# Optimization experiments

Measured on AMD Instinct MI355X. Metric: run time of the kernel, lower is better.

## Reference

```python
import jax, jax.numpy as jnp
import numpy as np

H = 256  # hidden_units
B = 64   # batch
D = 2048 # question length


def setup_inputs() -> dict:
    key = jax.random.key(0)
    ks = jax.random.split(key, 9)
    s = 1.0 / np.sqrt(H)
    return {
        "context": jax.random.normal(ks[0], (B, H), dtype=jnp.float32),
        "question": jax.random.normal(ks[1], (B, D, H), dtype=jnp.float32),
        "hidden": jax.random.normal(ks[2], (1, B, H), dtype=jnp.float32),
        "W1": jax.random.uniform(ks[3], (H, H), jnp.float32, -s, s),  # linear_g1, no bias
        "W2": jax.random.uniform(ks[4], (H, H), jnp.float32, -s, s),  # linear_g2
        "b2": jax.random.uniform(ks[5], (H,), jnp.float32, -s, s),
        "W3": jax.random.uniform(ks[6], (H, H), jnp.float32, -s, s),  # linear_g3, no bias
        "W4": jax.random.uniform(ks[7], (1, H), jnp.float32, -s, s),  # linear_g4
        "b4": jax.random.uniform(ks[8], (1,), jnp.float32, -s, s),
    }


def reference(context, question, hidden, W1, W2, b2, W3, W4, b4):
    # hidden: (1,B,H) -> (B,1,H); linear_g3 (no bias)
    g3 = jnp.swapaxes(hidden, 0, 1) @ W3.T            # (B,1,H)
    # linear_g2 on context, then unsqueeze(1)
    g2 = (context @ W2.T + b2)[:, None, :]            # (B,1,H)
    # linear_g1 on question (no bias)
    g1 = question @ W1.T                              # (B,D,H)
    # The torch repeat/view sequence is exactly a broadcast add in (B,D,H)
    s = jnp.tanh(g2 + g3 + g1)                        # (B,D,H)
    scores = s @ W4.T + b4                            # (B,D,1)
    attn = jax.nn.softmax(scores, axis=1)             # softmax over D
    # attn.transpose(1,2) bmm question -> (B,1,H)
    return jnp.einsum('bdo,bdh->boh', attn, question)
```

## Files before the change

kernel.cpp:

```cpp
#include <hip/hip_runtime.h>
#include <hip/hip_bf16.h>
#include <math.h>

#define HD 256
#define BB 64
#define DD 2048
#define NCHK 8
#define NST 4

typedef __attribute__((ext_vector_type(8))) short  short8;
typedef __attribute__((ext_vector_type(4))) float  float4v;
typedef __attribute__((ext_vector_type(4))) unsigned uint4v;
typedef __attribute__((ext_vector_type(4))) unsigned short ushort4v;

__device__ inline unsigned short f2bf(float f) {
    unsigned u = __builtin_bit_cast(unsigned, f);
    u += 0x7FFFu + ((u >> 16) & 1u);
    return (unsigned short)(u >> 16);
}
__device__ inline float bf2f(unsigned short u) {
    return __builtin_bit_cast(float, (unsigned)u << 16);
}

__device__ inline short8 cvt8(float4v lo, float4v hi) {
    uint4v u;
    asm("v_cvt_pk_bf16_f32 %0, %1, %2" : "=v"(u[0]) : "v"(lo[0]), "v"(lo[1]));
    asm("v_cvt_pk_bf16_f32 %0, %1, %2" : "=v"(u[1]) : "v"(lo[2]), "v"(lo[3]));
    asm("v_cvt_pk_bf16_f32 %0, %1, %2" : "=v"(u[2]) : "v"(hi[0]), "v"(hi[1]));
    asm("v_cvt_pk_bf16_f32 %0, %1, %2" : "=v"(u[3]) : "v"(hi[2]), "v"(hi[3]));
    return __builtin_bit_cast(short8, u);
}

__device__ inline float fast_exp2(float x) {
    float r;
    asm("v_exp_f32 %0, %1" : "=v"(r) : "v"(x));
    return r;
}
__device__ inline float fast_tanh(float x) {
    float y = x * 2.8853900817779268f;
    y = fminf(fmaxf(y, -30.f), 30.f);
    float t = fast_exp2(y);
    float r;
    asm("v_rcp_f32 %0, %1" : "=v"(r) : "v"(t + 1.f));
    return (t - 1.f) * r;
}

#define SYNC_LDS() do { asm volatile("s_waitcnt lgkmcnt(0)" ::: "memory"); \
                        __builtin_amdgcn_s_barrier(); \
                        asm volatile("" ::: "memory"); } while (0)

__global__ __launch_bounds__(256) void k_prep(const float* __restrict__ W1,
                                              unsigned short* __restrict__ w1b,
                                              const float* __restrict__ ctx,
                                              const float* __restrict__ hid,
                                              const float* __restrict__ W2,
                                              const float* __restrict__ b2,
                                              const float* __restrict__ W3,
                                              float* __restrict__ g23) {
    if (blockIdx.x < 64) {
        int i = blockIdx.x * 256 + threadIdx.x;
        float4v v = ((const float4v*)W1)[i];
        ushort4v o;
        o[0] = f2bf(v[0]); o[1] = f2bf(v[1]); o[2] = f2bf(v[2]); o[3] = f2bf(v[3]);
        ((ushort4v*)w1b)[i] = o;
    } else {
        int b = blockIdx.x - 64, t = threadIdx.x;
        __shared__ float c[HD], hh[HD];
        c[t]  = ctx[b * HD + t];
        hh[t] = hid[b * HD + t];
        __syncthreads();
        const float4v* w2 = (const float4v*)(W2 + (size_t)t * HD);
        const float4v* w3 = (const float4v*)(W3 + (size_t)t * HD);
        float acc = b2[t];
        #pragma unroll 8
        for (int k = 0; k < 64; ++k) {
            float4v a = w2[k], d = w3[k];
            int k4 = k * 4;
            acc += c[k4] * a[0] + c[k4 + 1] * a[1] + c[k4 + 2] * a[2] + c[k4 + 3] * a[3];
            acc += hh[k4] * d[0] + hh[k4 + 1] * d[1] + hh[k4 + 2] * d[2] + hh[k4 + 3] * d[3];
        }
        g23[b * HD + t] = acc;
    }
}

__global__ __launch_bounds__(512) void k_fused(const float* __restrict__ q,
                                               const unsigned short* __restrict__ w1b,
                                               const float* __restrict__ g23,
                                               const float* __restrict__ W4,
                                               float* __restrict__ pl,
                                               float* __restrict__ pO) {
    __shared__ __attribute__((aligned(16))) unsigned short buf0[64 * HD];
    __shared__ __attribute__((aligned(16))) unsigned short buf1[64 * HD];
    __shared__ float sp[8][64];
    __shared__ float g23s[HD], w4s[HD];

    const int t = threadIdx.x;
    const int chunk = blockIdx.x, b = blockIdx.y;
    const int lane = t & 63, wave = t >> 6;
    const int l15 = lane & 15, lk = lane >> 4;
    const int hb = wave * 32;
    const int cg = lane & 7, ro = lane >> 3;

    const float* qc = q + ((size_t)b * DD + chunk * 256) * HD;

    const int srow = t >> 5, schk = t & 31;
    const int swz = (srow & 7) << 4;

    float4v s0, s1, s2, s3, s4, s5, s6, s7;
    {
        const float* p0 = qc + (size_t)srow * HD + schk * 8;
        s0 = *(const float4v*)(p0);                s1 = *(const float4v*)(p0 + 4);
        s2 = *(const float4v*)(p0 + 16 * HD);      s3 = *(const float4v*)(p0 + 16 * HD + 4);
        s4 = *(const float4v*)(p0 + 32 * HD);      s5 = *(const float4v*)(p0 + 32 * HD + 4);
        s6 = *(const float4v*)(p0 + 48 * HD);      s7 = *(const float4v*)(p0 + 48 * HD + 4);
    }

    short8 bfr[8][2];
    #pragma unroll
    for (int kb = 0; kb < 8; ++kb)
        #pragma unroll
        for (int nf = 0; nf < 2; ++nf)
            bfr[kb][nf] = *(const short8*)&w1b[(size_t)(hb + nf * 16 + l15) * HD + kb * 32 + lk * 8];

    if (t < 256) g23s[t] = g23[b * HD + t];
    else         w4s[t - 256] = W4[t - 256];

    float l = 0.f;
    float4v O = {0.f, 0.f, 0.f, 0.f};

    #pragma unroll 1
    for (int ts = 0; ts < NST; ++ts) {
        unsigned short* cur = (ts & 1) ? buf1 : buf0;

        SYNC_LDS();

        {
            short8 p0 = cvt8(s0, s1);
            short8 p1 = cvt8(s2, s3);
            short8 p2 = cvt8(s4, s5);
            short8 p3 = cvt8(s6, s7);
            int base = srow * 512 + ((schk * 16) ^ swz);
            *(short8*)((char*)cur + base)              = p0;
            *(short8*)((char*)cur + base + 16 * 512)   = p1;
            *(short8*)((char*)cur + base + 32 * 512)   = p2;
            *(short8*)((char*)cur + base + 48 * 512)   = p3;
        }
        if (ts + 1 < NST) {
            const float* pn = qc + (size_t)((ts + 1) * 64 + srow) * HD + schk * 8;
            s0 = *(const float4v*)(pn);                s1 = *(const float4v*)(pn + 4);
            s2 = *(const float4v*)(pn + 16 * HD);      s3 = *(const float4v*)(pn + 16 * HD + 4);
            s4 = *(const float4v*)(pn + 32 * HD);      s5 = *(const float4v*)(pn + 32 * HD + 4);
            s6 = *(const float4v*)(pn + 48 * HD);      s7 = *(const float4v*)(pn + 48 * HD + 4);
        }
        SYNC_LDS();

        #pragma unroll
        for (int mf = 0; mf < 4; ++mf) {
            float4v acc0 = {0.f, 0.f, 0.f, 0.f}, acc1 = {0.f, 0.f, 0.f, 0.f};
            const int d = mf * 16 + l15;
            const int dsw = (d & 7) << 4;
            #pragma unroll
            for (int kb = 0; kb < 8; ++kb) {
                int byte = d * 512 + ((kb * 64 + lk * 16) ^ dsw);
                short8 bq = *(const short8*)((const char*)cur + byte);
                acc0 = __builtin_amdgcn_mfma_f32_16x16x32_bf16(bfr[kb][0], bq, acc0, 0, 0, 0);
                acc1 = __builtin_amdgcn_mfma_f32_16x16x32_bf16(bfr[kb][1], bq, acc1, 0, 0, 0);
            }
            float s = 0.f;
            {
                int h0 = hb + lk * 4;
                float4v g4 = *(const float4v*)&g23s[h0];
                float4v w4 = *(const float4v*)&w4s[h0];
                #pragma unroll
                for (int r = 0; r < 4; ++r) s += fast_tanh(acc0[r] + g4[r]) * w4[r];
            }
            {
                int h0 = hb + 16 + lk * 4;
                float4v g4 = *(const float4v*)&g23s[h0];
                float4v w4 = *(const float4v*)&w4s[h0];
                #pragma unroll
                for (int r = 0; r < 4; ++r) s += fast_tanh(acc1[r] + g4[r]) * w4[r];
            }
            s += __shfl_xor(s, 16, 64);
            s += __shfl_xor(s, 32, 64);
            if (lk == 0) sp[wave][mf * 16 + l15] = s;
        }
        SYNC_LDS();

        float sc = sp[0][lane] + sp[1][lane] + sp[2][lane] + sp[3][lane]
                 + sp[4][lane] + sp[5][lane] + sp[6][lane] + sp[7][lane];
        float w = fast_exp2(sc * 1.4426950408889634f);
        l += w;
        const int cb = wave * 64 + cg * 8;
        #pragma unroll
        for (int i = 0; i < 8; ++i) {
            int d = ro * 8 + i;
            float wd = __shfl(w, d, 64);
            int byte = d * 512 + (cb ^ ((d & 7) << 4));
            ushort4v v = *(const ushort4v*)((const char*)cur + byte);
            O[0] += wd * bf2f(v[0]);
            O[1] += wd * bf2f(v[1]);
            O[2] += wd * bf2f(v[2]);
            O[3] += wd * bf2f(v[3]);
        }
    }

    #pragma unroll
    for (int j = 0; j < 4; ++j) {
        O[j] += __shfl_xor(O[j], 8, 64);
        O[j] += __shfl_xor(O[j], 16, 64);
        O[j] += __shfl_xor(O[j], 32, 64);
    }
    if (ro == 0)
        *(float4v*)&pO[((size_t)(b * NCHK + chunk)) * HD + wave * 32 + cg * 4] = O;

    l += __shfl_xor(l, 1, 64);
    l += __shfl_xor(l, 2, 64);
    l += __shfl_xor(l, 4, 64);
    l += __shfl_xor(l, 8, 64);
    l += __shfl_xor(l, 16, 64);
    l += __shfl_xor(l, 32, 64);
    if (t == 0) pl[b * NCHK + chunk] = l;
}

__global__ __launch_bounds__(256) void k_comb(const float* __restrict__ pl,
                                              const float* __restrict__ pO,
                                              float* __restrict__ out) {
    int b = blockIdx.x, t = threadIdx.x;
    float L = 0.f;
    #pragma unroll
    for (int c = 0; c < NCHK; ++c) L += pl[b * NCHK + c];
    float s = 0.f;
    #pragma unroll
    for (int c = 0; c < NCHK; ++c) s += pO[((size_t)(b * NCHK + c)) * HD + t];
    out[b * HD + t] = s / L;
}

extern "C" void kernel_launch(void* const* d_in, const int* in_sizes, int n_in,
                              void* d_out, int out_size, void* d_ws, size_t ws_size,
                              hipStream_t stream) {
    (void)in_sizes; (void)n_in; (void)out_size; (void)ws_size;
    const float* ctx = (const float*)d_in[0];
    const float* q   = (const float*)d_in[1];
    const float* hid = (const float*)d_in[2];
    const float* W1  = (const float*)d_in[3];
    const float* W2  = (const float*)d_in[4];
    const float* b2  = (const float*)d_in[5];
    const float* W3  = (const float*)d_in[6];
    const float* W4  = (const float*)d_in[7];
    float* out = (float*)d_out;

    char* ws = (char*)d_ws;
    unsigned short* w1b = (unsigned short*)(ws);
    float* g23 = (float*)(ws + 131072);
    float* pl  = (float*)(ws + 196608);
    float* pO  = (float*)(ws + 198656);

    k_prep <<<dim3(128), dim3(256), 0, stream>>>(W1, w1b, ctx, hid, W2, b2, W3, g23);
    k_fused<<<dim3(NCHK, BB), dim3(512), 0, stream>>>(q, w1b, g23, W4, pl, pO);
    k_comb <<<dim3(BB), dim3(256), 0, stream>>>(pl, pO, out);
}
```

Baseline: 69.18 us.

## Single-buffer LDS tile, register-resident g23/W4, bf16 partial scores

Replaces the two bf16 LDS staging buffers with one tile, since each iteration is already bracketed by barriers. The g23 and W4 values each lane needs move from shared memory into registers loaded once before the loop. Per-wave partial scores are stored to LDS as packed bf16 and summed with two vector reads. The aim is a smaller LDS footprint, to allow more resident blocks per CU, and fewer LDS reads. In exchange it adds register pressure and rounds the per-wave partial scores to bf16 before the softmax, which costs accuracy.

```diff
diff --git a/kernel.cpp b/kernel.cpp
--- a/kernel.cpp
+++ b/kernel.cpp
@@ -89,10 +89,8 @@
                                                const float* __restrict__ W4,
                                                float* __restrict__ pl,
                                                float* __restrict__ pO) {
-    __shared__ __attribute__((aligned(16))) unsigned short buf0[64 * HD];
-    __shared__ __attribute__((aligned(16))) unsigned short buf1[64 * HD];
-    __shared__ float sp[8][64];
-    __shared__ float g23s[HD], w4s[HD];
+    __shared__ __attribute__((aligned(16))) unsigned short tile[64 * HD];
+    __shared__ __attribute__((aligned(16))) unsigned short spb[64][8];
 
     const int t = threadIdx.x;
     const int chunk = blockIdx.x, b = blockIdx.y;
@@ -122,16 +120,21 @@
         for (int nf = 0; nf < 2; ++nf)
             bfr[kb][nf] = *(const short8*)&w1b[(size_t)(hb + nf * 16 + l15) * HD + kb * 32 + lk * 8];
 
-    if (t < 256) g23s[t] = g23[b * HD + t];
-    else         w4s[t - 256] = W4[t - 256];
+    float gv[2][4], wv[2][4];
+    #pragma unroll
+    for (int nf = 0; nf < 2; ++nf)
+        #pragma unroll
+        for (int r = 0; r < 4; ++r) {
+            int h = hb + nf * 16 + lk * 4 + r;
+            gv[nf][r] = g23[b * HD + h];
+            wv[nf][r] = W4[h];
+        }
 
     float l = 0.f;
     float4v O = {0.f, 0.f, 0.f, 0.f};
 
     #pragma unroll 1
     for (int ts = 0; ts < NST; ++ts) {
-        unsigned short* cur = (ts & 1) ? buf1 : buf0;
-
         SYNC_LDS();
 
         {
@@ -140,10 +143,10 @@
             short8 p2 = cvt8(s4, s5);
             short8 p3 = cvt8(s6, s7);
             int base = srow * 512 + ((schk * 16) ^ swz);
-            *(short8*)((char*)cur + base)              = p0;
-            *(short8*)((char*)cur + base + 16 * 512)   = p1;
-            *(short8*)((char*)cur + base + 32 * 512)   = p2;
-            *(short8*)((char*)cur + base + 48 * 512)   = p3;
+            *(short8*)((char*)tile + base)              = p0;
+            *(short8*)((char*)tile + base + 16 * 512)   = p1;
+            *(short8*)((char*)tile + base + 32 * 512)   = p2;
+            *(short8*)((char*)tile + base + 48 * 512)   = p3;
         }
         if (ts + 1 < NST) {
             const float* pn = qc + (size_t)((ts + 1) * 64 + srow) * HD + schk * 8;
@@ -162,33 +165,28 @@
             #pragma unroll
             for (int kb = 0; kb < 8; ++kb) {
                 int byte = d * 512 + ((kb * 64 + lk * 16) ^ dsw);
-                short8 bq = *(const short8*)((const char*)cur + byte);
+                short8 bq = *(const short8*)((const char*)tile + byte);
                 acc0 = __builtin_amdgcn_mfma_f32_16x16x32_bf16(bfr[kb][0], bq, acc0, 0, 0, 0);
                 acc1 = __builtin_amdgcn_mfma_f32_16x16x32_bf16(bfr[kb][1], bq, acc1, 0, 0, 0);
             }
             float s = 0.f;
-            {
-                int h0 = hb + lk * 4;
-                float4v g4 = *(const float4v*)&g23s[h0];
-                float4v w4 = *(const float4v*)&w4s[h0];
-                #pragma unroll
-                for (int r = 0; r < 4; ++r) s += fast_tanh(acc0[r] + g4[r]) * w4[r];
-            }
-            {
-                int h0 = hb + 16 + lk * 4;
-                float4v g4 = *(const float4v*)&g23s[h0];
-                float4v w4 = *(const float4v*)&w4s[h0];
-                #pragma unroll
-                for (int r = 0; r < 4; ++r) s += fast_tanh(acc1[r] + g4[r]) * w4[r];
-            }
+            #pragma unroll
+            for (int r = 0; r < 4; ++r) s += fast_tanh(acc0[r] + gv[0][r]) * wv[0][r];
+            #pragma unroll
+            for (int r = 0; r < 4; ++r) s += fast_tanh(acc1[r] + gv[1][r]) * wv[1][r];
             s += __shfl_xor(s, 16, 64);
             s += __shfl_xor(s, 32, 64);
-            if (lk == 0) sp[wave][mf * 16 + l15] = s;
+            if (lk == 0) spb[mf * 16 + l15][wave] = f2bf(s);
         }
         SYNC_LDS();
 
-        float sc = sp[0][lane] + sp[1][lane] + sp[2][lane] + sp[3][lane]
-                 + sp[4][lane] + sp[5][lane] + sp[6][lane] + sp[7][lane];
+        float sc;
+        {
+            ushort4v a = *(const ushort4v*)&spb[lane][0];
+            ushort4v c = *(const ushort4v*)&spb[lane][4];
+            sc = bf2f(a[0]) + bf2f(a[1]) + bf2f(a[2]) + bf2f(a[3])
+               + bf2f(c[0]) + bf2f(c[1]) + bf2f(c[2]) + bf2f(c[3]);
+        }
         float w = fast_exp2(sc * 1.4426950408889634f);
         l += w;
         const int cb = wave * 64 + cg * 8;
@@ -197,7 +195,7 @@
             int d = ro * 8 + i;
             float wd = __shfl(w, d, 64);
             int byte = d * 512 + (cb ^ ((d & 7) << 4));
-            ushort4v v = *(const ushort4v*)((const char*)cur + byte);
+            ushort4v v = *(const ushort4v*)((const char*)tile + byte);
             O[0] += wd * bf2f(v[0]);
             O[1] += wd * bf2f(v[1]);
             O[2] += wd * bf2f(v[2]);
```

New measurement: 66.45 us. 4.0% less time.
